# Optimization experiments

Hardware: AMD Instinct MI355X
Metric: run time of the kernel (lower is better)

The kernel has to match this reference:

```python
import jax, jax.numpy as jnp
import numpy as np

N, E, D_IN, HID, D_OUT = 200000, 5000000, 128, 16, 2


def setup_inputs() -> dict:
    key = jax.random.key(0)
    ks = jax.random.split(key, 8)
    x = jax.random.normal(ks[0], (N, D_IN), dtype=jnp.float32)
    edge_index = jax.random.randint(ks[1], (2, E), 0, N, dtype=jnp.int32)
    W1 = jax.random.normal(ks[2], (D_IN, HID), dtype=jnp.float32) / np.sqrt(D_IN)
    b1 = jnp.zeros((HID,), dtype=jnp.float32)
    W3 = jax.random.normal(ks[3], (HID, HID), dtype=jnp.float32) / np.sqrt(HID)
    b3 = jnp.zeros((HID,), dtype=jnp.float32)
    W2 = jax.random.normal(ks[4], (HID, D_OUT), dtype=jnp.float32) / np.sqrt(HID)
    b2 = jnp.zeros((D_OUT,), dtype=jnp.float32)
    return {"x": x, "edge_index": edge_index, "W1": W1, "b1": b1,
            "W3": W3, "b3": b3, "W2": W2, "b2": b2}


def reference(x, edge_index, W1, b1, W3, b3, W2, b2):
    # GCNConv: add self-loops, symmetric normalization, aggregate, linear+bias.
    src, dst = edge_index[0], edge_index[1]
    loops = jnp.arange(N, dtype=src.dtype)
    src_f = jnp.concatenate([src, loops])  # [E+N]
    dst_f = jnp.concatenate([dst, loops])
    deg = jax.ops.segment_sum(jnp.ones_like(src_f, dtype=jnp.float32), dst_f,
                              num_segments=N)
    dis = jnp.where(deg > 0, jax.lax.rsqrt(jnp.maximum(deg, 1.0)), 0.0)
    norm = dis[src_f] * dis[dst_f]  # [E+N]

    def gcn_conv(h, W, b):
        h = h @ W                                   # [N, F_out] small GEMM
        msg = h[src_f] * norm[:, None]              # gather + scale
        agg = jax.ops.segment_sum(msg, dst_f, num_segments=N)  # scatter-add
        return agg + b

    h = jax.nn.relu(gcn_conv(x, W1, b1))    # conv1 (dropout is identity in eval)
    h = jax.nn.relu(gcn_conv(h, W3, b3))    # conv3 loop (conv_number-2 = 1 iter)
    h = gcn_conv(h, W2, b2)                 # conv2
    return jax.nn.log_softmax(h, axis=1)
```

## Files before the change

### kernel.cpp

```cpp
#include <hip/hip_runtime.h>

#define NN 200000
#define NE 5000000
#define DIN 128
#define HID 16
#define DOUT 2
#define BSZ 391
#define NB 512
#define LBITS 9
#define NCH 8
#define SLICE_DIV 25000
#define NK (NB * NCH)
#define NKB 512
#define SKEYS 4096
#define PB 256
#define PT 512

static_assert((size_t)NB * BSZ >= NN, "bucket coverage");
static_assert((NN - 1) / SLICE_DIV == NCH - 1, "slice count");


__global__ __launch_bounds__(PT) void hist_pass(const int* __restrict__ dst,
                                                int* __restrict__ blockHist) {
    __shared__ int h[NKB];
    for (int k = threadIdx.x; k < NKB; k += PT) h[k] = 0;
    __syncthreads();
    for (int i = blockIdx.x * PT + threadIdx.x; i < NE; i += PB * PT)
        atomicAdd(&h[dst[i] / BSZ], 1);
    __syncthreads();
    for (int k = threadIdx.x; k < NKB; k += PT)
        blockHist[(size_t)blockIdx.x * NKB + k] = h[k];
}

__global__ __launch_bounds__(256) void tot_pass(const int* __restrict__ blockHist,
                                                int* __restrict__ chunkStart) {
    int k = blockIdx.x * 256 + threadIdx.x;
    if (k >= NKB) return;
    int s = 0;
#pragma unroll 8
    for (int b = 0; b < PB; ++b) s += blockHist[(size_t)b * NKB + k];
    chunkStart[k] = s;
}

__global__ __launch_bounds__(NKB) void scan_keys(int* __restrict__ chunkStart) {
    __shared__ int wsum[8];
    int t = threadIdx.x;
    int lane = t & 63, w = t >> 6;
    int v = chunkStart[t];
    int inc = v;
    for (int off = 1; off < 64; off <<= 1) {
        int nb = __shfl_up(inc, off, 64);
        if (lane >= off) inc += nb;
    }
    if (lane == 63) wsum[w] = inc;
    __syncthreads();
    if (t == 0) {
        int car = 0;
#pragma unroll
        for (int i = 0; i < 8; ++i) { int u = wsum[i]; wsum[i] = car; car += u; }
    }
    __syncthreads();
    chunkStart[t] = inc - v + wsum[w];
    if (t == 0) chunkStart[NKB] = NE;
}

__global__ __launch_bounds__(256) void offsets_pass(int* __restrict__ blockHist,
                                                    const int* __restrict__ chunkStart) {
    int k = blockIdx.x * 256 + threadIdx.x;
    if (k >= NKB) return;
    int r = chunkStart[k];
#pragma unroll 8
    for (int b = 0; b < PB; ++b) {
        size_t idx = (size_t)b * NKB + k;
        int v = blockHist[idx];
        blockHist[idx] = r;
        r += v;
    }
}

__global__ __launch_bounds__(PT) void scatter_pass(const int* __restrict__ src,
                                                   const int* __restrict__ dst,
                                                   const int* __restrict__ blockHist,
                                                   unsigned* __restrict__ pedge) {
    __shared__ int cur[NKB];
    for (int k = threadIdx.x; k < NKB; k += PT)
        cur[k] = blockHist[(size_t)blockIdx.x * NKB + k];
    __syncthreads();
    for (int i = blockIdx.x * PT + threadIdx.x; i < NE; i += PB * PT) {
        int sv = src[i];
        int dv = dst[i];
        int bk = dv / BSZ;
        int pos = atomicAdd(&cur[bk], 1);
        pedge[pos] = ((unsigned)sv << LBITS) | (unsigned)(dv - bk * BSZ);
    }
}


__global__ __launch_bounds__(512) void subsort(const unsigned* __restrict__ pedge,
                                               const int* __restrict__ chunkStart,
                                               int* __restrict__ pedge2,
                                               int* __restrict__ rowStart,
                                               float* __restrict__ dis) {
    __shared__ int h[SKEYS];
    __shared__ int wsum[8];
    int t = threadIdx.x;
    int b = blockIdx.x;
    int lane = t & 63, w = t >> 6;
    int e0 = chunkStart[b], e1 = chunkStart[b + 1];
    for (int k = t; k < SKEYS; k += 512) h[k] = 0;
    __syncthreads();
    for (int i = e0 + t; i < e1; i += 512) {
        unsigned p = pedge[i];
        int sv = (int)(p >> LBITS);
        atomicAdd(&h[(sv / SLICE_DIV) * 512 + (p & 511u)], 1);
    }
    __syncthreads();
    if (t < BSZ) {
        int dg = 1;
#pragma unroll
        for (int s = 0; s < NCH; ++s) dg += h[s * 512 + t];
        int node = b * BSZ + t;
        if (node < NN) dis[node] = rsqrtf((float)dg);
    }
    int vals[8];
    int s = 0;
#pragma unroll
    for (int j = 0; j < 8; ++j) { vals[j] = h[t * 8 + j]; s += vals[j]; }
    int inc = s;
    for (int off = 1; off < 64; off <<= 1) {
        int nb = __shfl_up(inc, off, 64);
        if (lane >= off) inc += nb;
    }
    if (lane == 63) wsum[w] = inc;
    __syncthreads();
    if (t == 0) {
        int car = 0;
#pragma unroll
        for (int i = 0; i < 8; ++i) { int u = wsum[i]; wsum[i] = car; car += u; }
    }
    __syncthreads();
    int run = inc - s + wsum[w];
#pragma unroll
    for (int j = 0; j < 8; ++j) {
        int k = t * 8 + j;
        h[k] = run;
        int dl = k & 511, sl = k >> 9;
        if (dl < BSZ)
            rowStart[(size_t)(b * NCH + sl) * BSZ + dl] = e0 + run;
        run += vals[j];
    }
    __syncthreads();
    for (int i = e0 + t; i < e1; i += 512) {
        unsigned p = pedge[i];
        int sv = (int)(p >> LBITS);
        int key = (sv / SLICE_DIV) * 512 + (p & 511u);
        int pos = atomicAdd(&h[key], 1);
        pedge2[e0 + pos] = sv;
    }
    if (b == 0 && t == 0) rowStart[(size_t)NK * BSZ] = NE;
}


#define GXR 64
#define XPAD 132
__global__ __launch_bounds__(256) void gemm_x_w1(const float* __restrict__ x,
                                                 const float* __restrict__ W,
                                                 const float* __restrict__ dis,
                                                 float* __restrict__ out) {
    __shared__ float w[DIN * HID];
    __shared__ float xt[GXR * XPAD];
    int t = threadIdx.x;
    for (int i = t; i < DIN * HID; i += 256) w[i] = W[i];
    int rbase = blockIdx.x * GXR;
    const float4* xg = reinterpret_cast<const float4*>(x + (size_t)rbase * DIN);
    float4* xt4 = reinterpret_cast<float4*>(xt);
    for (int i = t; i < GXR * (DIN / 4); i += 256) {
        int row = i >> 5, kk = i & 31;
        xt4[row * (XPAD / 4) + kk] = xg[i];
    }
    __syncthreads();
    int row = t >> 2;
    int c0 = (t & 3) * 4;
    const float* xr = xt + row * XPAD;
    float ax = 0.f, ay = 0.f, az = 0.f, aw = 0.f;
#pragma unroll 4
    for (int k = 0; k < DIN; ++k) {
        float xv = xr[k];
        float4 wv = *reinterpret_cast<const float4*>(&w[k * HID + c0]);
        ax += xv * wv.x; ay += xv * wv.y; az += xv * wv.z; aw += xv * wv.w;
    }
    int node = rbase + row;
    float dd = dis[node];
    *reinterpret_cast<float4*>(&out[(size_t)node * HID + c0]) =
        make_float4(ax * dd, ay * dd, az * dd, aw * dd);
}

__global__ __launch_bounds__(256) void gemm_h_w16(const float* __restrict__ h,
                                                  const float* __restrict__ W,
                                                  const float* __restrict__ dis,
                                                  float* __restrict__ out) {
    __shared__ float w[HID * HID];
    if (threadIdx.x < HID * HID) w[threadIdx.x] = W[threadIdx.x];
    __syncthreads();
    int row = blockIdx.x * 16 + (threadIdx.x >> 4);
    int c = threadIdx.x & 15;
    if (row >= NN) return;
    const float4* hr = reinterpret_cast<const float4*>(h + (size_t)row * HID);
    float acc = 0.f;
#pragma unroll
    for (int k4 = 0; k4 < HID / 4; ++k4) {
        float4 v = hr[k4];
        acc += v.x * w[(4 * k4 + 0) * HID + c] + v.y * w[(4 * k4 + 1) * HID + c]
             + v.z * w[(4 * k4 + 2) * HID + c] + v.w * w[(4 * k4 + 3) * HID + c];
    }
    out[row * HID + c] = acc * dis[row];
}

__global__ __launch_bounds__(256) void gemm_h_w2(const float* __restrict__ h,
                                                 const float* __restrict__ W,
                                                 const float* __restrict__ dis,
                                                 float* __restrict__ out) {
    int t = blockIdx.x * 256 + threadIdx.x;
    int row = t >> 1;
    int c = t & 1;
    if (row >= NN) return;
    const float* hr = h + (size_t)row * HID;
    float acc = 0.f;
#pragma unroll
    for (int k = 0; k < HID; ++k) acc += hr[k] * W[k * DOUT + c];
    out[row * DOUT + c] = acc * dis[row];
}


__device__ __forceinline__ void acc_edges(const int* __restrict__ pedge2,
                                          const float4* __restrict__ xs4,
                                          int e, int e1, int c4, float4& a) {
    for (; e + 3 < e1; e += 4) {
        int s0 = pedge2[e], s1 = pedge2[e + 1];
        int s2 = pedge2[e + 2], s3 = pedge2[e + 3];
        float4 u0 = xs4[(s0 << 2) + c4];
        float4 u1 = xs4[(s1 << 2) + c4];
        float4 u2 = xs4[(s2 << 2) + c4];
        float4 u3 = xs4[(s3 << 2) + c4];
        a.x += (u0.x + u1.x) + (u2.x + u3.x);
        a.y += (u0.y + u1.y) + (u2.y + u3.y);
        a.z += (u0.z + u1.z) + (u2.z + u3.z);
        a.w += (u0.w + u1.w) + (u2.w + u3.w);
    }
    for (; e < e1; ++e) {
        float4 u = xs4[(pedge2[e] << 2) + c4];
        a.x += u.x; a.y += u.y; a.z += u.z; a.w += u.w;
    }
}

__global__ __launch_bounds__(1024, 8) void agg16_all(const int* __restrict__ pedge2,
                                                     const int* __restrict__ rowStart,
                                                     const float* __restrict__ xs,
                                                     const float* __restrict__ dis,
                                                     const float* __restrict__ bias,
                                                     float* __restrict__ buf,
                                                     int relu) {
    int t = threadIdx.x;
    int b = blockIdx.x;
    int base = b * BSZ;
    int c4 = t & 3;
    int q = t >> 2;
    int g0 = (q * BSZ) >> 8;
    int g1 = ((q + 1) * BSZ) >> 8;
    bool two = (g1 - g0) == 2;
    int n0 = base + g0, n1 = base + g0 + 1;
    bool v0 = n0 < NN;
    bool v1 = two && (n1 < NN);
    const float4* xs4 = reinterpret_cast<const float4*>(xs);
    float4* buf4 = reinterpret_cast<float4*>(buf);
    float4 a0 = make_float4(0.f, 0.f, 0.f, 0.f);
    float4 a1 = a0;
    if (v0) a0 = xs4[(n0 << 2) + c4];
    if (v1) a1 = xs4[(n1 << 2) + c4];
    for (int r = 0; r < NCH; ++r) {
        const int* rs = rowStart + (size_t)(b * NCH + r) * BSZ;
        if (v0) acc_edges(pedge2, xs4, rs[g0], rs[g0 + 1], c4, a0);
        if (v1) acc_edges(pedge2, xs4, rs[g0 + 1], rs[g0 + 2], c4, a1);
    }
    float4 bb = reinterpret_cast<const float4*>(bias)[c4];
    if (v0) {
        float dd = dis[n0];
        float4 v = make_float4(dd * a0.x + bb.x, dd * a0.y + bb.y,
                               dd * a0.z + bb.z, dd * a0.w + bb.w);
        if (relu) { v.x = fmaxf(v.x, 0.f); v.y = fmaxf(v.y, 0.f);
                    v.z = fmaxf(v.z, 0.f); v.w = fmaxf(v.w, 0.f); }
        buf4[(n0 << 2) + c4] = v;
    }
    if (v1) {
        float dd = dis[n1];
        float4 v = make_float4(dd * a1.x + bb.x, dd * a1.y + bb.y,
                               dd * a1.z + bb.z, dd * a1.w + bb.w);
        if (relu) { v.x = fmaxf(v.x, 0.f); v.y = fmaxf(v.y, 0.f);
                    v.z = fmaxf(v.z, 0.f); v.w = fmaxf(v.w, 0.f); }
        buf4[(n1 << 2) + c4] = v;
    }
}

__global__ __launch_bounds__(512) void agg2_lsm(const int* __restrict__ pedge2,
                                                const int* __restrict__ rowStart,
                                                const float* __restrict__ xs,
                                                const float* __restrict__ dis,
                                                const float* __restrict__ bias,
                                                float* __restrict__ out) {
    int t = threadIdx.x;
    int b = blockIdx.x;
    if (t >= BSZ) return;
    int node = b * BSZ + t;
    if (node >= NN) return;
    const float2* xs2 = reinterpret_cast<const float2*>(xs);
    float a0 = 0.f, a1 = 0.f;
    for (int s = 0; s < NCH; ++s) {
        const int* rs = rowStart + (size_t)(b * NCH + s) * BSZ;
        int e = rs[t], e1 = rs[t + 1];
        for (; e + 3 < e1; e += 4) {
            int s0 = pedge2[e], s1 = pedge2[e + 1];
            int s2 = pedge2[e + 2], s3 = pedge2[e + 3];
            float2 v0 = xs2[s0], v1 = xs2[s1], v2 = xs2[s2], v3 = xs2[s3];
            a0 += (v0.x + v1.x) + (v2.x + v3.x);
            a1 += (v0.y + v1.y) + (v2.y + v3.y);
        }
        for (; e < e1; ++e) {
            float2 v = xs2[pedge2[e]];
            a0 += v.x; a1 += v.y;
        }
    }
    float2 sv = xs2[node];
    float d = dis[node];
    float v0 = (a0 + sv.x) * d + bias[0];
    float v1 = (a1 + sv.y) * d + bias[1];
    float m = fmaxf(v0, v1);
    float lse = m + logf(__expf(v0 - m) + __expf(v1 - m));
    reinterpret_cast<float2*>(out)[node] = make_float2(v0 - lse, v1 - lse);
}


extern "C" void kernel_launch(void* const* d_in, const int* in_sizes, int n_in,
                              void* d_out, int out_size, void* d_ws, size_t ws_size,
                              hipStream_t stream) {
    const float* x = (const float*)d_in[0];
    const int* ei = (const int*)d_in[1];
    const float* W1 = (const float*)d_in[2];
    const float* b1 = (const float*)d_in[3];
    const float* W3 = (const float*)d_in[4];
    const float* b3 = (const float*)d_in[5];
    const float* W2 = (const float*)d_in[6];
    const float* b2 = (const float*)d_in[7];
    float* out = (float*)d_out;

    const int* src = ei;
    const int* dst = ei + NE;

    int* W = (int*)d_ws;
    unsigned* pedge = (unsigned*)W;
    int* pedge2 = W + NE;
    int* rowStart = W + 2 * (size_t)NE;
    int* blockHist = rowStart + (size_t)NK * BSZ + 4;
    int* chunkStart = blockHist + (size_t)PB * NKB;
    float* dis = (float*)(chunkStart + NKB + 4);
    float* bufB = dis + NN;
    float* bufA = (float*)W;

    const int B = 256;
    auto cdiv = [](long long a, long long b) { return (int)((a + b - 1) / b); };

    hist_pass<<<PB, PT, 0, stream>>>(dst, blockHist);
    tot_pass<<<cdiv(NKB, 256), 256, 0, stream>>>(blockHist, chunkStart);
    scan_keys<<<1, NKB, 0, stream>>>(chunkStart);
    offsets_pass<<<cdiv(NKB, 256), 256, 0, stream>>>(blockHist, chunkStart);
    scatter_pass<<<PB, PT, 0, stream>>>(src, dst, blockHist, pedge);
    subsort<<<NB, 512, 0, stream>>>(pedge, chunkStart, pedge2, rowStart, dis);

    gemm_x_w1<<<NN / GXR, B, 0, stream>>>(x, W1, dis, bufA);
    agg16_all<<<NB, 1024, 0, stream>>>(pedge2, rowStart, bufA, dis, b1, bufB, 1);

    gemm_h_w16<<<cdiv(NN, 16), B, 0, stream>>>(bufB, W3, dis, bufA);
    agg16_all<<<NB, 1024, 0, stream>>>(pedge2, rowStart, bufA, dis, b3, bufB, 1);

    gemm_h_w2<<<cdiv((long long)NN * DOUT, B), B, 0, stream>>>(bufB, W2, dis, bufA);
    agg2_lsm<<<NB, 512, 0, stream>>>(pedge2, rowStart, bufA, dis, b2, out);
}
```

Baseline: 305.6 us.

## Vectorize edge reads and restructure first GEMM to read x directly

Edge-index reads in the histogram and scatter passes use int4 loads, with four atomics per iteration and twice as many partition blocks. The first feature GEMM no longer stages x through shared memory: each thread loads float4 chunks of its row directly and uses 512-thread blocks. This aims to cut instruction overhead and LDS traffic. In exchange, the four threads sharing a row each read the full row, which leans on cache reuse.

```diff
diff --git a/kernel.cpp b/kernel.cpp
--- a/kernel.cpp
+++ b/kernel.cpp
@@ -13,20 +13,27 @@
 #define NK (NB * NCH)
 #define NKB 512
 #define SKEYS 4096
-#define PB 256
+#define PB 512
 #define PT 512
 
 static_assert((size_t)NB * BSZ >= NN, "bucket coverage");
 static_assert((NN - 1) / SLICE_DIV == NCH - 1, "slice count");
-
-
-__global__ __launch_bounds__(PT) void hist_pass(const int* __restrict__ dst,
+static_assert(NE % 4 == 0, "int4 edge reads");
+
+
+__global__ __launch_bounds__(PT) void hist_pass(const int4* __restrict__ dst4,
                                                 int* __restrict__ blockHist) {
     __shared__ int h[NKB];
     for (int k = threadIdx.x; k < NKB; k += PT) h[k] = 0;
     __syncthreads();
-    for (int i = blockIdx.x * PT + threadIdx.x; i < NE; i += PB * PT)
-        atomicAdd(&h[dst[i] / BSZ], 1);
+    const int NI = NE / 4;
+    for (int i = blockIdx.x * PT + threadIdx.x; i < NI; i += PB * PT) {
+        int4 d = dst4[i];
+        atomicAdd(&h[d.x / BSZ], 1);
+        atomicAdd(&h[d.y / BSZ], 1);
+        atomicAdd(&h[d.z / BSZ], 1);
+        atomicAdd(&h[d.w / BSZ], 1);
+    }
     __syncthreads();
     for (int k = threadIdx.x; k < NKB; k += PT)
         blockHist[(size_t)blockIdx.x * NKB + k] = h[k];
@@ -37,7 +44,7 @@
     int k = blockIdx.x * 256 + threadIdx.x;
     if (k >= NKB) return;
     int s = 0;
-#pragma unroll 8
+#pragma unroll 16
     for (int b = 0; b < PB; ++b) s += blockHist[(size_t)b * NKB + k];
     chunkStart[k] = s;
 }
@@ -78,20 +85,27 @@
     }
 }
 
-__global__ __launch_bounds__(PT) void scatter_pass(const int* __restrict__ src,
-                                                   const int* __restrict__ dst,
+__global__ __launch_bounds__(PT) void scatter_pass(const int4* __restrict__ src4,
+                                                   const int4* __restrict__ dst4,
                                                    const int* __restrict__ blockHist,
                                                    unsigned* __restrict__ pedge) {
     __shared__ int cur[NKB];
     for (int k = threadIdx.x; k < NKB; k += PT)
         cur[k] = blockHist[(size_t)blockIdx.x * NKB + k];
     __syncthreads();
-    for (int i = blockIdx.x * PT + threadIdx.x; i < NE; i += PB * PT) {
-        int sv = src[i];
-        int dv = dst[i];
-        int bk = dv / BSZ;
-        int pos = atomicAdd(&cur[bk], 1);
-        pedge[pos] = ((unsigned)sv << LBITS) | (unsigned)(dv - bk * BSZ);
+    const int NI = NE / 4;
+    for (int i = blockIdx.x * PT + threadIdx.x; i < NI; i += PB * PT) {
+        int4 s = src4[i];
+        int4 d = dst4[i];
+        int b0 = d.x / BSZ, b1 = d.y / BSZ, b2 = d.z / BSZ, b3 = d.w / BSZ;
+        int p0 = atomicAdd(&cur[b0], 1);
+        int p1 = atomicAdd(&cur[b1], 1);
+        int p2 = atomicAdd(&cur[b2], 1);
+        int p3 = atomicAdd(&cur[b3], 1);
+        pedge[p0] = ((unsigned)s.x << LBITS) | (unsigned)(d.x - b0 * BSZ);
+        pedge[p1] = ((unsigned)s.y << LBITS) | (unsigned)(d.y - b1 * BSZ);
+        pedge[p2] = ((unsigned)s.z << LBITS) | (unsigned)(d.z - b2 * BSZ);
+        pedge[p3] = ((unsigned)s.w << LBITS) | (unsigned)(d.w - b3 * BSZ);
     }
 }
 
@@ -161,37 +175,35 @@
 }
 
 
-#define GXR 64
-#define XPAD 132
-__global__ __launch_bounds__(256) void gemm_x_w1(const float* __restrict__ x,
+#define GXT 512
+#define GXR 128
+__global__ __launch_bounds__(GXT) void gemm_x_w1(const float* __restrict__ x,
                                                  const float* __restrict__ W,
                                                  const float* __restrict__ dis,
                                                  float* __restrict__ out) {
     __shared__ float w[DIN * HID];
-    __shared__ float xt[GXR * XPAD];
-    int t = threadIdx.x;
-    for (int i = t; i < DIN * HID; i += 256) w[i] = W[i];
-    int rbase = blockIdx.x * GXR;
-    const float4* xg = reinterpret_cast<const float4*>(x + (size_t)rbase * DIN);
-    float4* xt4 = reinterpret_cast<float4*>(xt);
-    for (int i = t; i < GXR * (DIN / 4); i += 256) {
-        int row = i >> 5, kk = i & 31;
-        xt4[row * (XPAD / 4) + kk] = xg[i];
-    }
-    __syncthreads();
-    int row = t >> 2;
+    int t = threadIdx.x;
+    for (int i = t; i < DIN * HID; i += GXT) w[i] = W[i];
+    __syncthreads();
+    int row = blockIdx.x * GXR + (t >> 2);
     int c0 = (t & 3) * 4;
-    const float* xr = xt + row * XPAD;
+    if (row >= NN) return;
+    const float4* xr = reinterpret_cast<const float4*>(x + (size_t)row * DIN);
     float ax = 0.f, ay = 0.f, az = 0.f, aw = 0.f;
-#pragma unroll 4
-    for (int k = 0; k < DIN; ++k) {
-        float xv = xr[k];
-        float4 wv = *reinterpret_cast<const float4*>(&w[k * HID + c0]);
-        ax += xv * wv.x; ay += xv * wv.y; az += xv * wv.z; aw += xv * wv.w;
-    }
-    int node = rbase + row;
-    float dd = dis[node];
-    *reinterpret_cast<float4*>(&out[(size_t)node * HID + c0]) =
+#pragma unroll
+    for (int k4 = 0; k4 < DIN / 4; ++k4) {
+        float4 xv = xr[k4];
+        float4 w0 = *reinterpret_cast<const float4*>(&w[(4 * k4 + 0) * HID + c0]);
+        float4 w1 = *reinterpret_cast<const float4*>(&w[(4 * k4 + 1) * HID + c0]);
+        float4 w2 = *reinterpret_cast<const float4*>(&w[(4 * k4 + 2) * HID + c0]);
+        float4 w3 = *reinterpret_cast<const float4*>(&w[(4 * k4 + 3) * HID + c0]);
+        ax += xv.x * w0.x + xv.y * w1.x + xv.z * w2.x + xv.w * w3.x;
+        ay += xv.x * w0.y + xv.y * w1.y + xv.z * w2.y + xv.w * w3.y;
+        az += xv.x * w0.z + xv.y * w1.z + xv.z * w2.z + xv.w * w3.z;
+        aw += xv.x * w0.w + xv.y * w1.w + xv.z * w2.w + xv.w * w3.w;
+    }
+    float dd = dis[row];
+    *reinterpret_cast<float4*>(&out[(size_t)row * HID + c0]) =
         make_float4(ax * dd, ay * dd, az * dd, aw * dd);
 }
 
@@ -352,8 +364,8 @@
     const float* b2 = (const float*)d_in[7];
     float* out = (float*)d_out;
 
-    const int* src = ei;
-    const int* dst = ei + NE;
+    const int4* src4 = (const int4*)ei;
+    const int4* dst4 = (const int4*)(ei + NE);
 
     int* W = (int*)d_ws;
     unsigned* pedge = (unsigned*)W;
@@ -368,14 +380,14 @@
     const int B = 256;
     auto cdiv = [](long long a, long long b) { return (int)((a + b - 1) / b); };
 
-    hist_pass<<<PB, PT, 0, stream>>>(dst, blockHist);
+    hist_pass<<<PB, PT, 0, stream>>>(dst4, blockHist);
     tot_pass<<<cdiv(NKB, 256), 256, 0, stream>>>(blockHist, chunkStart);
     scan_keys<<<1, NKB, 0, stream>>>(chunkStart);
     offsets_pass<<<cdiv(NKB, 256), 256, 0, stream>>>(blockHist, chunkStart);
-    scatter_pass<<<PB, PT, 0, stream>>>(src, dst, blockHist, pedge);
+    scatter_pass<<<PB, PT, 0, stream>>>(src4, dst4, blockHist, pedge);
     subsort<<<NB, 512, 0, stream>>>(pedge, chunkStart, pedge2, rowStart, dis);
 
-    gemm_x_w1<<<NN / GXR, B, 0, stream>>>(x, W1, dis, bufA);
+    gemm_x_w1<<<cdiv(NN, GXR), GXT, 0, stream>>>(x, W1, dis, bufA);
     agg16_all<<<NB, 1024, 0, stream>>>(pedge2, rowStart, bufA, dis, b1, bufB, 1);
 
     gemm_h_w16<<<cdiv(NN, 16), B, 0, stream>>>(bufB, W3, dis, bufA);
```

New measurement: 301.9 us. Within noise of the previous version (-1.2%).
